# Performance work log

Measured on AMD Instinct MI355X. Metric: run time of the kernel, lower is better.

Reference implementation:

```python
import jax, jax.numpy as jnp
import numpy as np
import math

D_MODEL = 1024
N_HEADS = 16
GEOM_DIM = 7
B, S = 4, 1024


def setup_inputs() -> dict:
    key = jax.random.key(0)
    ks = jax.random.split(key, 12)
    w = lambda k, shape: (jax.random.normal(k, shape, dtype=jnp.float32) * 0.02)
    return {
        "x": jax.random.normal(ks[0], (B, S, D_MODEL), dtype=jnp.float32),
        "geom_feat": jax.random.normal(ks[1], (B, S, S, GEOM_DIM), dtype=jnp.float32),
        "mask": jax.random.randint(ks[2], (B, S), 0, 2, dtype=jnp.int32),
        "Wq": w(ks[3], (D_MODEL, D_MODEL)), "bq": jnp.zeros((D_MODEL,), jnp.float32),
        "Wk": w(ks[4], (D_MODEL, D_MODEL)), "bk": jnp.zeros((D_MODEL,), jnp.float32),
        "Wv": w(ks[5], (D_MODEL, D_MODEL)), "bv": jnp.zeros((D_MODEL,), jnp.float32),
        "Wo": w(ks[6], (D_MODEL, D_MODEL)), "bo": jnp.zeros((D_MODEL,), jnp.float32),
        "Wg": w(ks[7], (GEOM_DIM, N_HEADS)), "bg": jnp.zeros((N_HEADS,), jnp.float32),
    }


def reference(x, geom_feat, mask, Wq, bq, Wk, bk, Wv, bv, Wo, bo, Wg, bg):
    b, s, d = x.shape
    h = Wg.shape[1]
    dk = d // h
    scale = math.sqrt(dk)
    # QKV projections -> [b, h, s, dk]
    Q = (x @ Wq + bq).reshape(b, s, h, dk).transpose(0, 2, 1, 3)
    K = (x @ Wk + bk).reshape(b, s, h, dk).transpose(0, 2, 1, 3)
    V = (x @ Wv + bv).reshape(b, s, h, dk).transpose(0, 2, 1, 3)
    # attention scores [b, h, s, s]
    scores = jnp.einsum("bhqd,bhkd->bhqk", Q, K) / scale
    # geometric structure bias: [b,s,s,geom_dim] -> [b,s,s,h] -> [b,h,s,s]
    struct_bias = (geom_feat @ Wg + bg).transpose(0, 3, 1, 2)
    scores = scores + struct_bias
    # key-padding mask [b, s] -> [b, 1, 1, s]
    scores = jnp.where(mask[:, None, None, :] == 0, -10000.0, scores)
    attn = jax.nn.softmax(scores, axis=-1)  # dropout disabled (eval / p=0)
    ctx = jnp.einsum("bhqk,bhkd->bhqd", attn, V)
    ctx = ctx.transpose(0, 2, 1, 3).reshape(b, s, d)
    return ctx @ Wo + bo
```

## Files before the change

kernel.cpp:

```cpp
#include <hip/hip_runtime.h>
#include <hip/hip_bf16.h>
#include <math.h>

#define BB 4
#define SS 1024
#define DD 1024
#define NH 16
#define DK 64
#define GD 7

typedef _Float16 half8 __attribute__((ext_vector_type(8)));
typedef _Float16 half4v __attribute__((ext_vector_type(4)));
typedef float floatx4 __attribute__((ext_vector_type(4)));

__device__ inline half8 cvt8(const float4 a, const float4 b) {
  half8 h;
  h[0] = (_Float16)a.x; h[1] = (_Float16)a.y; h[2] = (_Float16)a.z; h[3] = (_Float16)a.w;
  h[4] = (_Float16)b.x; h[5] = (_Float16)b.y; h[6] = (_Float16)b.z; h[7] = (_Float16)b.w;
  return h;
}

__global__ __launch_bounds__(256) void prep(const float* __restrict__ x,
                                            _Float16* __restrict__ xh,
                                            const float* __restrict__ Wq,
                                            const float* __restrict__ Wk,
                                            const float* __restrict__ Wv,
                                            const float* __restrict__ Wo,
                                            _Float16* __restrict__ Wt) {
  __shared__ _Float16 Tl[64 * 72];
  const int t = threadIdx.x;
  if (blockIdx.x < 2048) {
    const int i = blockIdx.x * 256 + t;
    const float4 a = ((const float4*)x)[i * 2];
    const float4 b = ((const float4*)x)[i * 2 + 1];
    ((half8*)xh)[i] = cvt8(a, b);
    return;
  }
  const int pf = blockIdx.x - 2048;
  const int z = pf >> 8, rem = pf & 255;
  const int n0 = (rem >> 4) * 64, k0 = (rem & 15) * 64;
  const float* src = (z == 0) ? Wq : (z == 1) ? Wk : (z == 2) ? Wv : Wo;
#pragma unroll
  for (int i = 0; i < 4; ++i) {
    const int u = i * 256 + t;
    const int r = u >> 4, c4 = (u & 15) * 4;
    const float4 v = *(const float4*)(src + (size_t)(k0 + r) * DD + n0 + c4);
    Tl[(c4 + 0) * 72 + r] = (_Float16)v.x;
    Tl[(c4 + 1) * 72 + r] = (_Float16)v.y;
    Tl[(c4 + 2) * 72 + r] = (_Float16)v.z;
    Tl[(c4 + 3) * 72 + r] = (_Float16)v.w;
  }
  __syncthreads();
  _Float16* dst = Wt + (size_t)z * DD * DD;
#pragma unroll
  for (int i = 0; i < 2; ++i) {
    const int u = i * 256 + t;
    const int nr = u >> 3, ks = u & 7;
    const half8 hv = *(const half8*)&Tl[nr * 72 + ks * 8];
    *(half8*)(dst + (size_t)(n0 + nr) * DD + k0 + ks * 8) = hv;
  }
}

template <bool PRE>
__global__ __launch_bounds__(256) void fused0(const _Float16* __restrict__ A,
                                              const _Float16* __restrict__ Bt,
                                              const float* __restrict__ bq,
                                              const float* __restrict__ bk,
                                              const float* __restrict__ bv,
                                              _Float16* __restrict__ Oq,
                                              _Float16* __restrict__ Ok,
                                              _Float16* __restrict__ Ov,
                                              const float* __restrict__ geom,
                                              const int* __restrict__ mask,
                                              const float* __restrict__ Wg,
                                              const float* __restrict__ bg,
                                              unsigned char* __restrict__ bias8) {
  const int t = threadIdx.x;
  int role, idx;
  if (PRE) {
    const int g = blockIdx.x, grp = g / 11, rem = g % 11;
    if (rem < 3) { role = 0; idx = grp * 3 + rem; }
    else         { role = 1; idx = grp * 8 + rem - 3; }
  } else {
    role = 0; idx = blockIdx.x;
  }

  if (role == 0) {
    __shared__ _Float16 Als[128 * 72];
    __shared__ _Float16 Bls[128 * 72];
    const int w = t >> 6, lane = t & 63, quad = lane >> 4, col = lane & 15;
    const int m0 = (idx & 31) * 128, n0 = (idx >> 5) * 128;
    const int mw = (w >> 1) * 64, nw = (w & 1) * 64;
    const floatx4 zero4 = {0.f, 0.f, 0.f, 0.f};
    floatx4 acc[4][4];
#pragma unroll
    for (int i = 0; i < 4; ++i)
#pragma unroll
      for (int j = 0; j < 4; ++j) acc[i][j] = zero4;

    for (int k0 = 0; k0 < DD; k0 += 64) {
#pragma unroll
      for (int i = 0; i < 4; ++i) {
        const int u = i * 256 + t;
        const int row = u >> 3, seg = u & 7;
        const half8 hv = *(const half8*)(A + (size_t)(m0 + row) * DD + k0 + seg * 8);
        *(half8*)&Als[row * 72 + seg * 8] = hv;
      }
#pragma unroll
      for (int i = 0; i < 4; ++i) {
        const int u = i * 256 + t;
        const int row = u >> 3, seg = u & 7;
        const half8 hv = *(const half8*)(Bt + (size_t)(n0 + row) * DD + k0 + seg * 8);
        *(half8*)&Bls[row * 72 + seg * 8] = hv;
      }
      __syncthreads();
#pragma unroll
      for (int kk = 0; kk < 2; ++kk) {
        half8 af[4], bf[4];
        const int u = (quad + kk * 4) * 8;
#pragma unroll
        for (int i = 0; i < 4; ++i)
          af[i] = *(const half8*)&Als[(mw + i * 16 + col) * 72 + u];
#pragma unroll
        for (int j = 0; j < 4; ++j)
          bf[j] = *(const half8*)&Bls[(nw + j * 16 + col) * 72 + u];
#pragma unroll
        for (int i = 0; i < 4; ++i)
#pragma unroll
          for (int j = 0; j < 4; ++j)
            acc[i][j] =
                __builtin_amdgcn_mfma_f32_16x16x32_f16(af[i], bf[j], acc[i][j], 0, 0, 0);
      }
      __syncthreads();
    }

#pragma unroll
    for (int j = 0; j < 4; ++j) {
      const int n = n0 + nw + j * 16 + col;
      const int which = n >> 10, hd = n & 1023;
      const int h = hd >> 6, d = hd & 63;
      const float* bp = (which == 0) ? bq : (which == 1) ? bk : bv;
      const float bias = bp[hd];
      _Float16* ob = (which == 0) ? Oq : (which == 1) ? Ok : Ov;
#pragma unroll
      for (int i = 0; i < 4; ++i) {
#pragma unroll
        for (int reg = 0; reg < 4; ++reg) {
          const int m = m0 + mw + i * 16 + quad * 4 + reg;
          const int b = m >> 10, s = m & 1023;
          ob[(((size_t)b * NH + h) * SS + s) * DK + d] = (_Float16)(acc[i][j][reg] + bias);
        }
      }
    }
    return;
  }

  if constexpr (PRE) {
    __shared__ float wgL[GD * NH + NH];
    const int r = idx;
    const int b = r >> 9;
    const int q = (r & 511) * 2 + (t >> 7);
    const int k8 = (t & 127) * 8;
    if (t < GD * NH) wgL[t] = Wg[t];
    if (t < NH) wgL[GD * NH + t] = bg[t];

    const float* gp = geom + ((size_t)b * SS + q) * SS * GD + (size_t)k8 * GD;
    float4 gv[14];
#pragma unroll
    for (int i = 0; i < 14; ++i) gv[i] = *(const float4*)(gp + i * 4);
    const float* gf = (const float*)gv;

    const int4 m4a = *(const int4*)(mask + b * SS + k8);
    const int4 m4b = *(const int4*)(mask + b * SS + k8 + 4);
    const int mk[8] = {m4a.x, m4a.y, m4a.z, m4a.w, m4b.x, m4b.y, m4b.z, m4b.w};

    __syncthreads();

    unsigned char* dst = bias8 + ((size_t)b * NH * SS + q) * SS + k8;
#pragma unroll
    for (int h = 0; h < NH; ++h) {
      float wg[GD];
#pragma unroll
      for (int g = 0; g < GD; ++g) wg[g] = wgL[g * NH + h];
      const float bgh = wgL[GD * NH + h];
      float bi[8];
#pragma unroll
      for (int k2 = 0; k2 < 8; ++k2) {
        float s = bgh;
#pragma unroll
        for (int g = 0; g < GD; ++g) s = fmaf(gf[k2 * GD + g], wg[g], s);
        bi[k2] = mk[k2] ? s : -100.f;
      }
      int w0 = 0, w1 = 0;
      w0 = __builtin_amdgcn_cvt_pk_fp8_f32(bi[0], bi[1], w0, false);
      w0 = __builtin_amdgcn_cvt_pk_fp8_f32(bi[2], bi[3], w0, true);
      w1 = __builtin_amdgcn_cvt_pk_fp8_f32(bi[4], bi[5], w1, false);
      w1 = __builtin_amdgcn_cvt_pk_fp8_f32(bi[6], bi[7], w1, true);
      uint2 u2v;
      u2v.x = (unsigned)w0;
      u2v.y = (unsigned)w1;
      *(uint2*)(dst + (size_t)h * SS * SS) = u2v;
    }
  }
}

__global__ __launch_bounds__(256) void hgemm1(const _Float16* __restrict__ A,
                                              const _Float16* __restrict__ Bt,
                                              const float* __restrict__ b0,
                                              float* __restrict__ Of) {
  __shared__ _Float16 Als[128 * 72];
  __shared__ _Float16 Bls[128 * 72];
  const int t = threadIdx.x;
  const int w = t >> 6, lane = t & 63, quad = lane >> 4, col = lane & 15;
  const int m0 = blockIdx.x * 128, n0 = blockIdx.y * 128;
  const int mw = (w >> 1) * 64, nw = (w & 1) * 64;
  const floatx4 zero4 = {0.f, 0.f, 0.f, 0.f};
  floatx4 acc[4][4];
#pragma unroll
  for (int i = 0; i < 4; ++i)
#pragma unroll
    for (int j = 0; j < 4; ++j) acc[i][j] = zero4;

  for (int k0 = 0; k0 < DD; k0 += 64) {
#pragma unroll
    for (int i = 0; i < 4; ++i) {
      const int u = i * 256 + t;
      const int row = u >> 3, seg = u & 7;
      const half8 hv = *(const half8*)(A + (size_t)(m0 + row) * DD + k0 + seg * 8);
      *(half8*)&Als[row * 72 + seg * 8] = hv;
    }
#pragma unroll
    for (int i = 0; i < 4; ++i) {
      const int u = i * 256 + t;
      const int row = u >> 3, seg = u & 7;
      const half8 hv = *(const half8*)(Bt + (size_t)(n0 + row) * DD + k0 + seg * 8);
      *(half8*)&Bls[row * 72 + seg * 8] = hv;
    }
    __syncthreads();
#pragma unroll
    for (int kk = 0; kk < 2; ++kk) {
      half8 af[4], bf[4];
      const int u = (quad + kk * 4) * 8;
#pragma unroll
      for (int i = 0; i < 4; ++i) af[i] = *(const half8*)&Als[(mw + i * 16 + col) * 72 + u];
#pragma unroll
      for (int j = 0; j < 4; ++j) bf[j] = *(const half8*)&Bls[(nw + j * 16 + col) * 72 + u];
#pragma unroll
      for (int i = 0; i < 4; ++i)
#pragma unroll
        for (int j = 0; j < 4; ++j)
          acc[i][j] = __builtin_amdgcn_mfma_f32_16x16x32_f16(af[i], bf[j], acc[i][j], 0, 0, 0);
    }
    __syncthreads();
  }

#pragma unroll
  for (int j = 0; j < 4; ++j) {
    const int n = n0 + nw + j * 16 + col;
    const float bias = b0[n];
#pragma unroll
    for (int i = 0; i < 4; ++i) {
#pragma unroll
      for (int reg = 0; reg < 4; ++reg) {
        const int m = m0 + mw + i * 16 + quad * 4 + reg;
        Of[(size_t)m * DD + n] = acc[i][j][reg] + bias;
      }
    }
  }
}

template <bool PREBIAS>
__global__ __launch_bounds__(256) void attn(const _Float16* __restrict__ Q,
                                            const _Float16* __restrict__ K,
                                            const _Float16* __restrict__ V,
                                            const unsigned char* __restrict__ bias8,
                                            const float* __restrict__ geom,
                                            const int* __restrict__ mask,
                                            const float* __restrict__ Wg,
                                            const float* __restrict__ bg,
                                            _Float16* __restrict__ ctxbuf) {
  __shared__ _Float16 Ks[64 * 64];
  __shared__ _Float16 Vt[64 * 72];
  __shared__ unsigned char biasL[PREBIAS ? 64 * 80 : 64 * 144];
  __shared__ _Float16 pL[4 * 16 * 72];
  __shared__ unsigned char mskL[SS];

  const int t = threadIdx.x;
  const int w = t >> 6, lane = t & 63, quad = lane >> 4, col = lane & 15;
  const int h = blockIdx.x, qt = blockIdx.y, b = blockIdx.z;
  const int q0 = qt * 64;
  const size_t bh = (size_t)b * NH + h;
  const _Float16* Qb = Q + bh * SS * DK;
  const _Float16* Kb = K + bh * SS * DK;
  const _Float16* Vb = V + bh * SS * DK;
  _Float16* biasLf = (_Float16*)biasL;

  {
    const int j = t >> 2, u2 = (t & 3) * 2;
    const half8 h0 = *(const half8*)(Qb + (size_t)(q0 + j) * DK + u2 * 8);
    const half8 h1 = *(const half8*)(Qb + (size_t)(q0 + j) * DK + u2 * 8 + 8);
    *(half8*)&Ks[(j * 8 + (u2 ^ (j & 7))) * 8] = h0;
    *(half8*)&Ks[(j * 8 + ((u2 + 1) ^ (j & 7))) * 8] = h1;
  }
  if constexpr (!PREBIAS) {
    const int4 m4 = *(const int4*)(mask + b * SS + t * 4);
    mskL[t * 4 + 0] = m4.x != 0;
    mskL[t * 4 + 1] = m4.y != 0;
    mskL[t * 4 + 2] = m4.z != 0;
    mskL[t * 4 + 3] = m4.w != 0;
  }
  __syncthreads();
  half8 qfrag[2];
  {
    const int qrow = w * 16 + col;
#pragma unroll
    for (int kk = 0; kk < 2; ++kk) {
      const int u = quad + kk * 4;
      qfrag[kk] = *(const half8*)&Ks[(qrow * 8 + (u ^ (qrow & 7))) * 8];
    }
  }

  float wgv[GD];
  float bgh = 0.f;
  const float* gptr = nullptr;
  if constexpr (!PREBIAS) {
#pragma unroll
    for (int g = 0; g < GD; ++g) wgv[g] = Wg[g * NH + h];
    bgh = bg[h];
    gptr = geom + (((size_t)b * SS + (q0 + (t >> 2))) * SS + (t & 3) * 16) * GD;
  }
  const unsigned char* bb8 = nullptr;
  if constexpr (PREBIAS) bb8 = bias8 + (bh * SS + q0) * SS;

  const floatx4 zero4 = {0.f, 0.f, 0.f, 0.f};
  floatx4 ctx[4] = {zero4, zero4, zero4, zero4};
  float lsum[4] = {0.f, 0.f, 0.f, 0.f};
  _Float16* pW = &pL[w * 16 * 72];

  for (int c = 0; c < 16; ++c) {
    const int k0 = c * 64;
    __syncthreads();

    {
      const int j = t >> 2, u2 = (t & 3) * 2;
      const half8 h0 = *(const half8*)(Kb + (size_t)(k0 + j) * DK + u2 * 8);
      const half8 h1 = *(const half8*)(Kb + (size_t)(k0 + j) * DK + u2 * 8 + 8);
      *(half8*)&Ks[(j * 8 + (u2 ^ (j & 7))) * 8] = h0;
      *(half8*)&Ks[(j * 8 + ((u2 + 1) ^ (j & 7))) * 8] = h1;
    }
    {
      const int kg = (t >> 4) * 4, dg = (t & 15) * 4;
      half4v f[4];
#pragma unroll
      for (int e = 0; e < 4; ++e)
        f[e] = *(const half4v*)(Vb + (size_t)(k0 + kg + e) * DK + dg);
#pragma unroll
      for (int i = 0; i < 4; ++i) {
        half4v hv = {f[0][i], f[1][i], f[2][i], f[3][i]};
        *(half4v*)&Vt[(dg + i) * 72 + kg] = hv;
      }
    }
    if constexpr (PREBIAS) {
      const int row = t >> 2, seg = (t & 3) * 16;
      const uint4 v = *(const uint4*)(bb8 + (size_t)row * SS + k0 + seg);
      *(uint4*)&biasL[row * 80 + seg] = v;
    } else {
      const int gq = t >> 2, gk = (t & 3) * 16;
#pragma unroll
      for (int sg = 0; sg < 4; ++sg) {
        float4 gvv[7];
#pragma unroll
        for (int i7 = 0; i7 < 7; ++i7) gvv[i7] = *(const float4*)(gptr + sg * 28 + i7 * 4);
        const float* gf = (const float*)gvv;
        half4v bv;
#pragma unroll
        for (int k2 = 0; k2 < 4; ++k2) {
          float bi = bgh;
#pragma unroll
          for (int g = 0; g < GD; ++g) bi = fmaf(gf[k2 * GD + g], wgv[g], bi);
          bv[k2] = mskL[k0 + gk + sg * 4 + k2] ? (_Float16)bi : (_Float16)(-100.f);
        }
        *(half4v*)&biasLf[gq * 72 + gk + sg * 4] = bv;
      }
      gptr += 64 * GD;
    }
    __syncthreads();

    floatx4 sc[4] = {zero4, zero4, zero4, zero4};
#pragma unroll
    for (int nt = 0; nt < 4; ++nt) {
      const int key = nt * 16 + col;
#pragma unroll
      for (int kk = 0; kk < 2; ++kk) {
        const int u = quad + kk * 4;
        const half8 kf = *(const half8*)&Ks[(key * 8 + (u ^ (key & 7))) * 8];
        sc[nt] = __builtin_amdgcn_mfma_f32_16x16x32_f16(qfrag[kk], kf, sc[nt], 0, 0, 0);
      }
    }

#pragma unroll
    for (int nt = 0; nt < 4; ++nt) {
#pragma unroll
      for (int reg = 0; reg < 4; ++reg) {
        const int q = quad * 4 + reg;
        float bias;
        if constexpr (PREBIAS) {
          bias = __builtin_amdgcn_cvt_f32_fp8(
              (int)biasL[(w * 16 + q) * 80 + nt * 16 + col], 0);
        } else {
          bias = (float)biasLf[(w * 16 + q) * 72 + nt * 16 + col];
        }
        const float s = fmaf(sc[nt][reg], 0.125f, bias);
        const float p = __expf(s);
        lsum[reg] += p;
        pW[q * 72 + nt * 16 + col] = (_Float16)p;
      }
    }

#pragma unroll
    for (int kk = 0; kk < 2; ++kk) {
      const half8 pa = *(const half8*)&pW[col * 72 + quad * 8 + kk * 32];
#pragma unroll
      for (int nt = 0; nt < 4; ++nt) {
        const half8 vb = *(const half8*)&Vt[(nt * 16 + col) * 72 + quad * 8 + kk * 32];
        ctx[nt] = __builtin_amdgcn_mfma_f32_16x16x32_f16(pa, vb, ctx[nt], 0, 0, 0);
      }
    }
  }

  float inv[4];
#pragma unroll
  for (int reg = 0; reg < 4; ++reg) {
    float l = lsum[reg];
    l += __shfl_xor(l, 1, 64);
    l += __shfl_xor(l, 2, 64);
    l += __shfl_xor(l, 4, 64);
    l += __shfl_xor(l, 8, 64);
    inv[reg] = 1.f / l;
  }
#pragma unroll
  for (int nt = 0; nt < 4; ++nt) {
#pragma unroll
    for (int reg = 0; reg < 4; ++reg) {
      const int q = q0 + w * 16 + quad * 4 + reg;
      ctxbuf[((size_t)b * SS + q) * DD + h * DK + nt * 16 + col] =
          (_Float16)(ctx[nt][reg] * inv[reg]);
    }
  }
}

extern "C" void kernel_launch(void* const* d_in, const int* in_sizes, int n_in,
                              void* d_out, int out_size, void* d_ws, size_t ws_size,
                              hipStream_t stream) {
  const float* x    = (const float*)d_in[0];
  const float* geom = (const float*)d_in[1];
  const int*   mask = (const int*)d_in[2];
  const float* Wq   = (const float*)d_in[3];
  const float* bq   = (const float*)d_in[4];
  const float* Wk   = (const float*)d_in[5];
  const float* bk   = (const float*)d_in[6];
  const float* Wv   = (const float*)d_in[7];
  const float* bv   = (const float*)d_in[8];
  const float* Wo   = (const float*)d_in[9];
  const float* bo   = (const float*)d_in[10];
  const float* Wg   = (const float*)d_in[11];
  const float* bg   = (const float*)d_in[12];
  float* out = (float*)d_out;

  const size_t NEL = (size_t)BB * SS * DD;
  char* p = (char*)d_ws;
  _Float16* xh   = (_Float16*)p;            p += NEL * 2;
  _Float16* Wt   = (_Float16*)p;            p += NEL * 2;
  _Float16* Qh   = (_Float16*)p;            p += NEL * 2;
  _Float16* Kh   = (_Float16*)p;            p += NEL * 2;
  _Float16* Vh   = (_Float16*)p;            p += NEL * 2;
  _Float16* ctxh = (_Float16*)p;            p += NEL * 2;
  unsigned char* bias8 = (unsigned char*)p;
  const size_t need = (size_t)48 * 1024 * 1024 + (size_t)BB * NH * SS * SS;
  const bool prebias = ws_size >= need;

  prep<<<3072, 256, 0, stream>>>(x, xh, Wq, Wk, Wv, Wo, Wt);

  if (prebias) {
    fused0<true><<<2816, 256, 0, stream>>>(xh, Wt, bq, bk, bv, Qh, Kh, Vh,
                                           geom, mask, Wg, bg, bias8);
    attn<true><<<dim3(NH, SS / 64, BB), 256, 0, stream>>>(Qh, Kh, Vh, bias8, geom, mask,
                                                          Wg, bg, ctxh);
  } else {
    fused0<false><<<768, 256, 0, stream>>>(xh, Wt, bq, bk, bv, Qh, Kh, Vh,
                                           geom, mask, Wg, bg, nullptr);
    attn<false><<<dim3(NH, SS / 64, BB), 256, 0, stream>>>(Qh, Kh, Vh, nullptr, geom, mask,
                                                           Wg, bg, ctxh);
  }

  hgemm1<<<dim3(32, 8), 256, 0, stream>>>(ctxh, Wt + (size_t)3 * DD * DD, bo, out);
}
```

Before: 338.1 us.

## Use async global-to-LDS loads with XOR swizzle and keep P in registers

GEMM tiles and attention Q/K tiles are now loaded with global_load_lds direct-to-LDS copies into an unpadded XOR-swizzled layout, replacing register-staged loads into padded LDS. In attention, the MFMA operands are swapped so S^T lands in registers and the probabilities feed the PV MFMA directly, removing the per-wave P round-trip through LDS. The change also vectorizes the bias reads and the context stores, and permutes the V transpose layout to match. The swapped operand layout and the permutation are subtle, and a mistake in either would break correctness.

Measured after the change: 322.5 us. -4.6%, faster.

```diff
diff --git a/kernel.cpp b/kernel.cpp
--- a/kernel.cpp
+++ b/kernel.cpp
@@ -12,6 +12,12 @@
 typedef _Float16 half8 __attribute__((ext_vector_type(8)));
 typedef _Float16 half4v __attribute__((ext_vector_type(4)));
 typedef float floatx4 __attribute__((ext_vector_type(4)));
+
+__device__ __forceinline__ void async_cp16(const void* g, void* l) {
+  __builtin_amdgcn_global_load_lds(
+      (const __attribute__((address_space(1))) void*)g,
+      (__attribute__((address_space(3))) void*)l, 16, 0, 0);
+}
 
 __device__ inline half8 cvt8(const float4 a, const float4 b) {
   half8 h;
@@ -86,11 +92,13 @@
   }
 
   if (role == 0) {
-    __shared__ _Float16 Als[128 * 72];
-    __shared__ _Float16 Bls[128 * 72];
+    __shared__ _Float16 Als[128 * 64];
+    __shared__ _Float16 Bls[128 * 64];
     const int w = t >> 6, lane = t & 63, quad = lane >> 4, col = lane & 15;
     const int m0 = (idx & 31) * 128, n0 = (idx >> 5) * 128;
     const int mw = (w >> 1) * 64, nw = (w & 1) * 64;
+    const int lr = lane >> 3, ls = lane & 7;
+    const int swz8 = (ls ^ lr) * 8;
     const floatx4 zero4 = {0.f, 0.f, 0.f, 0.f};
     floatx4 acc[4][4];
 #pragma unroll
@@ -98,32 +106,27 @@
 #pragma unroll
       for (int j = 0; j < 4; ++j) acc[i][j] = zero4;
 
+    const _Float16* aBase = A + (size_t)(m0 + lr) * DD + swz8;
+    const _Float16* bBase = Bt + (size_t)(n0 + lr) * DD + swz8;
+
     for (int k0 = 0; k0 < DD; k0 += 64) {
 #pragma unroll
-      for (int i = 0; i < 4; ++i) {
-        const int u = i * 256 + t;
-        const int row = u >> 3, seg = u & 7;
-        const half8 hv = *(const half8*)(A + (size_t)(m0 + row) * DD + k0 + seg * 8);
-        *(half8*)&Als[row * 72 + seg * 8] = hv;
-      }
-#pragma unroll
-      for (int i = 0; i < 4; ++i) {
-        const int u = i * 256 + t;
-        const int row = u >> 3, seg = u & 7;
-        const half8 hv = *(const half8*)(Bt + (size_t)(n0 + row) * DD + k0 + seg * 8);
-        *(half8*)&Bls[row * 72 + seg * 8] = hv;
+      for (int it = 0; it < 4; ++it) {
+        const int rb = it * 32 + w * 8;
+        async_cp16(aBase + (size_t)rb * DD + k0, &Als[rb * 64]);
+        async_cp16(bBase + (size_t)rb * DD + k0, &Bls[rb * 64]);
       }
       __syncthreads();
 #pragma unroll
       for (int kk = 0; kk < 2; ++kk) {
         half8 af[4], bf[4];
-        const int u = (quad + kk * 4) * 8;
+        const int sz = ((quad + kk * 4) ^ (col & 7)) * 8;
 #pragma unroll
         for (int i = 0; i < 4; ++i)
-          af[i] = *(const half8*)&Als[(mw + i * 16 + col) * 72 + u];
+          af[i] = *(const half8*)&Als[(mw + i * 16 + col) * 64 + sz];
 #pragma unroll
         for (int j = 0; j < 4; ++j)
-          bf[j] = *(const half8*)&Bls[(nw + j * 16 + col) * 72 + u];
+          bf[j] = *(const half8*)&Bls[(nw + j * 16 + col) * 64 + sz];
 #pragma unroll
         for (int i = 0; i < 4; ++i)
 #pragma unroll
@@ -208,12 +211,14 @@
                                               const _Float16* __restrict__ Bt,
                                               const float* __restrict__ b0,
                                               float* __restrict__ Of) {
-  __shared__ _Float16 Als[128 * 72];
-  __shared__ _Float16 Bls[128 * 72];
+  __shared__ _Float16 Als[128 * 64];
+  __shared__ _Float16 Bls[128 * 64];
   const int t = threadIdx.x;
   const int w = t >> 6, lane = t & 63, quad = lane >> 4, col = lane & 15;
   const int m0 = blockIdx.x * 128, n0 = blockIdx.y * 128;
   const int mw = (w >> 1) * 64, nw = (w & 1) * 64;
+  const int lr = lane >> 3, ls = lane & 7;
+  const int swz8 = (ls ^ lr) * 8;
   const floatx4 zero4 = {0.f, 0.f, 0.f, 0.f};
   floatx4 acc[4][4];
 #pragma unroll
@@ -221,30 +226,25 @@
 #pragma unroll
     for (int j = 0; j < 4; ++j) acc[i][j] = zero4;
 
+  const _Float16* aBase = A + (size_t)(m0 + lr) * DD + swz8;
+  const _Float16* bBase = Bt + (size_t)(n0 + lr) * DD + swz8;
+
   for (int k0 = 0; k0 < DD; k0 += 64) {
 #pragma unroll
-    for (int i = 0; i < 4; ++i) {
-      const int u = i * 256 + t;
-      const int row = u >> 3, seg = u & 7;
-      const half8 hv = *(const half8*)(A + (size_t)(m0 + row) * DD + k0 + seg * 8);
-      *(half8*)&Als[row * 72 + seg * 8] = hv;
-    }
-#pragma unroll
-    for (int i = 0; i < 4; ++i) {
-      const int u = i * 256 + t;
-      const int row = u >> 3, seg = u & 7;
-      const half8 hv = *(const half8*)(Bt + (size_t)(n0 + row) * DD + k0 + seg * 8);
-      *(half8*)&Bls[row * 72 + seg * 8] = hv;
+    for (int it = 0; it < 4; ++it) {
+      const int rb = it * 32 + w * 8;
+      async_cp16(aBase + (size_t)rb * DD + k0, &Als[rb * 64]);
+      async_cp16(bBase + (size_t)rb * DD + k0, &Bls[rb * 64]);
     }
     __syncthreads();
 #pragma unroll
     for (int kk = 0; kk < 2; ++kk) {
       half8 af[4], bf[4];
-      const int u = (quad + kk * 4) * 8;
-#pragma unroll
-      for (int i = 0; i < 4; ++i) af[i] = *(const half8*)&Als[(mw + i * 16 + col) * 72 + u];
-#pragma unroll
-      for (int j = 0; j < 4; ++j) bf[j] = *(const half8*)&Bls[(nw + j * 16 + col) * 72 + u];
+      const int sz = ((quad + kk * 4) ^ (col & 7)) * 8;
+#pragma unroll
+      for (int i = 0; i < 4; ++i) af[i] = *(const half8*)&Als[(mw + i * 16 + col) * 64 + sz];
+#pragma unroll
+      for (int j = 0; j < 4; ++j) bf[j] = *(const half8*)&Bls[(nw + j * 16 + col) * 64 + sz];
 #pragma unroll
       for (int i = 0; i < 4; ++i)
 #pragma unroll
@@ -282,7 +282,6 @@
   __shared__ _Float16 Ks[64 * 64];
   __shared__ _Float16 Vt[64 * 72];
   __shared__ unsigned char biasL[PREBIAS ? 64 * 80 : 64 * 144];
-  __shared__ _Float16 pL[4 * 16 * 72];
   __shared__ unsigned char mskL[SS];
 
   const int t = threadIdx.x;
@@ -295,12 +294,15 @@
   const _Float16* Vb = V + bh * SS * DK;
   _Float16* biasLf = (_Float16*)biasL;
 
+  const int lr = lane >> 3, ls = lane & 7;
+  const int swz8 = (ls ^ lr) * 8;
+
   {
-    const int j = t >> 2, u2 = (t & 3) * 2;
-    const half8 h0 = *(const half8*)(Qb + (size_t)(q0 + j) * DK + u2 * 8);
-    const half8 h1 = *(const half8*)(Qb + (size_t)(q0 + j) * DK + u2 * 8 + 8);
-    *(half8*)&Ks[(j * 8 + (u2 ^ (j & 7))) * 8] = h0;
-    *(half8*)&Ks[(j * 8 + ((u2 + 1) ^ (j & 7))) * 8] = h1;
+#pragma unroll
+    for (int it = 0; it < 2; ++it) {
+      const int rb = it * 32 + w * 8;
+      async_cp16(Qb + (size_t)(q0 + rb + lr) * DK + swz8, &Ks[rb * 64]);
+    }
   }
   if constexpr (!PREBIAS) {
     const int4 m4 = *(const int4*)(mask + b * SS + t * 4);
@@ -314,10 +316,8 @@
   {
     const int qrow = w * 16 + col;
 #pragma unroll
-    for (int kk = 0; kk < 2; ++kk) {
-      const int u = quad + kk * 4;
-      qfrag[kk] = *(const half8*)&Ks[(qrow * 8 + (u ^ (qrow & 7))) * 8];
-    }
+    for (int kk = 0; kk < 2; ++kk)
+      qfrag[kk] = *(const half8*)&Ks[qrow * 64 + (((quad + kk * 4) ^ (col & 7)) * 8)];
   }
 
   float wgv[GD];
@@ -334,35 +334,36 @@
 
   const floatx4 zero4 = {0.f, 0.f, 0.f, 0.f};
   floatx4 ctx[4] = {zero4, zero4, zero4, zero4};
-  float lsum[4] = {0.f, 0.f, 0.f, 0.f};
-  _Float16* pW = &pL[w * 16 * 72];
+  float lsum = 0.f;
+
+  const int kg = (t >> 4) * 4, dg = (t & 15) * 4;
+  const int cg = (kg & 0x20) | ((kg & 0x0C) << 1) | ((kg & 0x10) >> 2);
 
   for (int c = 0; c < 16; ++c) {
-    const int k0 = c * 64;
+    const int k0c = c * 64;
     __syncthreads();
 
     {
-      const int j = t >> 2, u2 = (t & 3) * 2;
-      const half8 h0 = *(const half8*)(Kb + (size_t)(k0 + j) * DK + u2 * 8);
-      const half8 h1 = *(const half8*)(Kb + (size_t)(k0 + j) * DK + u2 * 8 + 8);
-      *(half8*)&Ks[(j * 8 + (u2 ^ (j & 7))) * 8] = h0;
-      *(half8*)&Ks[(j * 8 + ((u2 + 1) ^ (j & 7))) * 8] = h1;
+#pragma unroll
+      for (int it = 0; it < 2; ++it) {
+        const int rb = it * 32 + w * 8;
+        async_cp16(Kb + (size_t)(k0c + rb + lr) * DK + swz8, &Ks[rb * 64]);
+      }
     }
     {
-      const int kg = (t >> 4) * 4, dg = (t & 15) * 4;
       half4v f[4];
 #pragma unroll
       for (int e = 0; e < 4; ++e)
-        f[e] = *(const half4v*)(Vb + (size_t)(k0 + kg + e) * DK + dg);
+        f[e] = *(const half4v*)(Vb + (size_t)(k0c + kg + e) * DK + dg);
 #pragma unroll
       for (int i = 0; i < 4; ++i) {
         half4v hv = {f[0][i], f[1][i], f[2][i], f[3][i]};
-        *(half4v*)&Vt[(dg + i) * 72 + kg] = hv;
+        *(half4v*)&Vt[(dg + i) * 72 + cg] = hv;
       }
     }
     if constexpr (PREBIAS) {
       const int row = t >> 2, seg = (t & 3) * 16;
-      const uint4 v = *(const uint4*)(bb8 + (size_t)row * SS + k0 + seg);
+      const uint4 v = *(const uint4*)(bb8 + (size_t)row * SS + k0c + seg);
       *(uint4*)&biasL[row * 80 + seg] = v;
     } else {
       const int gq = t >> 2, gk = (t & 3) * 16;
@@ -378,7 +379,7 @@
           float bi = bgh;
 #pragma unroll
           for (int g = 0; g < GD; ++g) bi = fmaf(gf[k2 * GD + g], wgv[g], bi);
-          bv[k2] = mskL[k0 + gk + sg * 4 + k2] ? (_Float16)bi : (_Float16)(-100.f);
+          bv[k2] = mskL[k0c + gk + sg * 4 + k2] ? (_Float16)bi : (_Float16)(-100.f);
         }
         *(half4v*)&biasLf[gq * 72 + gk + sg * 4] = bv;
       }
@@ -392,60 +393,67 @@
       const int key = nt * 16 + col;
 #pragma unroll
       for (int kk = 0; kk < 2; ++kk) {
-        const int u = quad + kk * 4;
-        const half8 kf = *(const half8*)&Ks[(key * 8 + (u ^ (key & 7))) * 8];
-        sc[nt] = __builtin_amdgcn_mfma_f32_16x16x32_f16(qfrag[kk], kf, sc[nt], 0, 0, 0);
-      }
-    }
-
+        const half8 kf = *(const half8*)&Ks[key * 64 + (((quad + kk * 4) ^ (col & 7)) * 8)];
+        sc[nt] = __builtin_amdgcn_mfma_f32_16x16x32_f16(kf, qfrag[kk], sc[nt], 0, 0, 0);
+      }
+    }
+
+    float ps[4][4];
 #pragma unroll
     for (int nt = 0; nt < 4; ++nt) {
+      float bias4[4];
+      if constexpr (PREBIAS) {
+        const unsigned bw =
+            *(const unsigned*)&biasL[(w * 16 + col) * 80 + nt * 16 + quad * 4];
+        bias4[0] = __builtin_amdgcn_cvt_f32_fp8((int)bw, 0);
+        bias4[1] = __builtin_amdgcn_cvt_f32_fp8((int)bw, 1);
+        bias4[2] = __builtin_amdgcn_cvt_f32_fp8((int)bw, 2);
+        bias4[3] = __builtin_amdgcn_cvt_f32_fp8((int)bw, 3);
+      } else {
+#pragma unroll
+        for (int reg = 0; reg < 4; ++reg)
+          bias4[reg] = (float)biasLf[(w * 16 + col) * 72 + nt * 16 + quad * 4 + reg];
+      }
 #pragma unroll
       for (int reg = 0; reg < 4; ++reg) {
-        const int q = quad * 4 + reg;
-        float bias;
-        if constexpr (PREBIAS) {
-          bias = __builtin_amdgcn_cvt_f32_fp8(
-              (int)biasL[(w * 16 + q) * 80 + nt * 16 + col], 0);
-        } else {
-          bias = (float)biasLf[(w * 16 + q) * 72 + nt * 16 + col];
-        }
-        const float s = fmaf(sc[nt][reg], 0.125f, bias);
+        const float s = fmaf(sc[nt][reg], 0.125f, bias4[reg]);
         const float p = __expf(s);
-        lsum[reg] += p;
-        pW[q * 72 + nt * 16 + col] = (_Float16)p;
+        lsum += p;
+        ps[nt][reg] = p;
       }
     }
 
 #pragma unroll
     for (int kk = 0; kk < 2; ++kk) {
-      const half8 pa = *(const half8*)&pW[col * 72 + quad * 8 + kk * 32];
+      half8 pf;
+      pf[0] = (_Float16)ps[2 * kk][0];
+      pf[1] = (_Float16)ps[2 * kk][1];
+      pf[2] = (_Float16)ps[2 * kk][2];
+      pf[3] = (_Float16)ps[2 * kk][3];
+      pf[4] = (_Float16)ps[2 * kk + 1][0];
+      pf[5] = (_Float16)ps[2 * kk + 1][1];
+      pf[6] = (_Float16)ps[2 * kk + 1][2];
+      pf[7] = (_Float16)ps[2 * kk + 1][3];
 #pragma unroll
       for (int nt = 0; nt < 4; ++nt) {
         const half8 vb = *(const half8*)&Vt[(nt * 16 + col) * 72 + quad * 8 + kk * 32];
-        ctx[nt] = __builtin_amdgcn_mfma_f32_16x16x32_f16(pa, vb, ctx[nt], 0, 0, 0);
-      }
-    }
-  }
-
-  float inv[4];
-#pragma unroll
-  for (int reg = 0; reg < 4; ++reg) {
-    float l = lsum[reg];
-    l += __shfl_xor(l, 1, 64);
-    l += __shfl_xor(l, 2, 64);
-    l += __shfl_xor(l, 4, 64);
-    l += __shfl_xor(l, 8, 64);
-    inv[reg] = 1.f / l;
-  }
+        ctx[nt] = __builtin_amdgcn_mfma_f32_16x16x32_f16(vb, pf, ctx[nt], 0, 0, 0);
+      }
+    }
+  }
+
+  float l = lsum;
+  l += __shfl_xor(l, 16, 64);
+  l += __shfl_xor(l, 32, 64);
+  const float inv = 1.f / l;
+
+  _Float16* op = ctxbuf + ((size_t)b * SS + q0 + w * 16 + col) * DD + h * DK + quad * 4;
 #pragma unroll
   for (int nt = 0; nt < 4; ++nt) {
-#pragma unroll
-    for (int reg = 0; reg < 4; ++reg) {
-      const int q = q0 + w * 16 + quad * 4 + reg;
-      ctxbuf[((size_t)b * SS + q) * DD + h * DK + nt * 16 + col] =
-          (_Float16)(ctx[nt][reg] * inv[reg]);
-    }
+    half4v o;
+#pragma unroll
+    for (int reg = 0; reg < 4; ++reg) o[reg] = (_Float16)(ctx[nt][reg] * inv);
+    *(half4v*)(op + nt * 16) = o;
   }
 }
 
```
